# Kernel optimization log

Measured on AMD Instinct MI355X. Metric: run time of the kernel, lower is better.

The kernel has to match this reference:

```python
import jax, jax.numpy as jnp
import numpy as np

B, T, H = 2, 2048, 1024
EXPAND, N = 2, 16
DIN = H * EXPAND  # 2048
EPS = 1e-6


def rmsnorm(x, w):
    var = jnp.mean(x * x, axis=-1, keepdims=True)
    return x * jax.lax.rsqrt(var + EPS) * w


def setup_inputs() -> dict:
    key = jax.random.key(0)
    ks = jax.random.split(key, 9)
    s_h = 1.0 / np.sqrt(H)
    s_d = 1.0 / np.sqrt(DIN)
    return {
        "x": jax.random.normal(ks[0], (B, T, H), jnp.float32),
        "norm_w": jnp.ones((H,), jnp.float32),
        "in_proj_w": jax.random.normal(ks[1], (H, 2 * DIN), jnp.float32) * s_h,
        "A_proj_w": jax.random.normal(ks[2], (DIN, DIN), jnp.float32) * s_d,
        "A_proj_b": jax.random.normal(ks[3], (DIN,), jnp.float32) * 0.02,
        "A_base": jnp.log(jnp.arange(1, N + 1, dtype=jnp.float32)),
        "B_proj_w": jax.random.normal(ks[4], (DIN, N), jnp.float32) * s_d,
        "C_proj_w": jax.random.normal(ks[5], (DIN, N), jnp.float32) * s_d,
        "D": jnp.ones((DIN,), jnp.float32),
        "out_proj_w": jax.random.normal(ks[6], (DIN, H), jnp.float32) * s_d,
    }


def liquid_scan(x_in, a_mod, a_base, B_in, C_in):
    # x_in, a_mod: [B,T,DIN]; B_in, C_in: [B,T,N]; a_base: [N]
    def step(h, inp):
        a_t, b_t, c_t, x_t = inp  # [B,DIN], [B,N], [B,N], [B,DIN]
        # h: [B, DIN, N]
        h = (a_t[:, :, None] * a_base) * h + b_t[:, None, :] * x_t[:, :, None]
        y_t = jnp.einsum('bdn,bn->bd', h, c_t)
        return h, y_t

    h0 = jnp.zeros((x_in.shape[0], DIN, N), x_in.dtype)
    xs = (jnp.swapaxes(a_mod, 0, 1), jnp.swapaxes(B_in, 0, 1),
          jnp.swapaxes(C_in, 0, 1), jnp.swapaxes(x_in, 0, 1))
    _, ys = jax.lax.scan(step, h0, xs)  # ys: [T,B,DIN]
    return jnp.swapaxes(ys, 0, 1)


def reference(x, norm_w, in_proj_w, A_proj_w, A_proj_b, A_base, B_proj_w, C_proj_w, D, out_proj_w):
    residual = x
    xn = rmsnorm(x, norm_w)
    xz = xn @ in_proj_w                      # [B,T,2*DIN]
    x_in, z = jnp.split(xz, 2, axis=-1)
    x_in = jax.nn.silu(x_in)
    a_mod = jax.nn.sigmoid(x_in @ A_proj_w + A_proj_b)  # [B,T,DIN]
    a_base = jax.nn.sigmoid(A_base)                      # [N]
    B_in = x_in @ B_proj_w                               # [B,T,N]
    C_in = x_in @ C_proj_w                               # [B,T,N]
    y = liquid_scan(x_in, a_mod, a_base, B_in, C_in)     # [B,T,DIN]
    y = (y + D * x_in) * jax.nn.silu(z)
    return residual + y @ out_proj_w
```

## Files before the change

### kernel.cpp

```cpp
#include <hip/hip_runtime.h>
#include <hip/hip_fp16.h>
#include <cstdint>

#define B_    2
#define T_    2048
#define H_    1024
#define DIN_  2048
#define NS_   16
#define M_    (B_*T_)
#define NCHUNK 64
#define LCHUNK 32

using bf16x8 = __attribute__((ext_vector_type(8))) short;
using f32x4  = __attribute__((ext_vector_type(4))) float;

__device__ __forceinline__ unsigned short f2bf(float f) {
    union { float f; uint32_t u; } x; x.f = f;
    uint32_t u = x.u;
    uint32_t r = (u + 0x7fffu + ((u >> 16) & 1u)) >> 16;
    return (unsigned short)r;
}
__device__ __forceinline__ float bf2f(unsigned short h) {
    union { uint32_t u; float f; } x; x.u = ((uint32_t)h) << 16;
    return x.f;
}
__device__ __forceinline__ float sigm(float v) { return 1.0f / (1.0f + expf(-v)); }
__device__ __forceinline__ float silu(float v) { return v / (1.0f + expf(-v)); }

__device__ __forceinline__ void gload_lds16(const void* g, void* l) {
    __builtin_amdgcn_global_load_lds(
        (__attribute__((address_space(1))) void*)(void*)g,
        (__attribute__((address_space(3))) void*)l, 16, 0, 0);
}

__global__ __launch_bounds__(256)
void prep_weights(const float* __restrict__ in_proj, const float* __restrict__ A_proj,
                  const float* __restrict__ out_proj,
                  unsigned short* __restrict__ inT, unsigned short* __restrict__ W2,
                  unsigned short* __restrict__ outT) {
    int bid = blockIdx.x;
    int tid = threadIdx.x;
    const float* src; unsigned short* dst; int K, N, l;
    if (bid < 4096)      { src = in_proj;  dst = inT;  K = 1024; N = 4096; l = bid; }
    else if (bid < 8192) { src = A_proj;   dst = W2;   K = 2048; N = 2048; l = bid - 4096; }
    else                 { src = out_proj; dst = outT; K = 2048; N = 1024; l = bid - 8192; }
    int ntiles = N >> 5;
    int n0 = (l % ntiles) * 32, k0 = (l / ntiles) * 32;
    __shared__ float tile[32][33];
    int tx = tid & 31, ty = tid >> 5;
#pragma unroll
    for (int i = 0; i < 32; i += 8)
        tile[ty + i][tx] = src[(size_t)(k0 + ty + i) * N + (n0 + tx)];
    __syncthreads();
    int sx = (tid & 15) * 2;
    int sy = tid >> 4;
#pragma unroll
    for (int i = 0; i < 32; i += 16) {
        int n = sy + i;
        float v0 = tile[sx][n], v1 = tile[sx + 1][n];
        size_t o = (size_t)(n0 + n) * K + (k0 + sx);
        *(ushort2*)&dst[o] = make_ushort2(f2bf(v0), f2bf(v1));
    }
}

__global__ __launch_bounds__(256)
void rmsnorm_bf(const float* __restrict__ x, const float* __restrict__ w,
                unsigned short* __restrict__ xh) {
    int row = blockIdx.x;
    int tid = threadIdx.x;
    const float4* xr = (const float4*)(x + (size_t)row * H_);
    float4 v = xr[tid];
    float ss = v.x * v.x + v.y * v.y + v.z * v.z + v.w * v.w;
#pragma unroll
    for (int o = 32; o > 0; o >>= 1) ss += __shfl_down(ss, o, 64);
    __shared__ float red[4];
    int lane = tid & 63, wv = tid >> 6;
    if (lane == 0) red[wv] = ss;
    __syncthreads();
    float tot = red[0] + red[1] + red[2] + red[3];
    float rstd = rsqrtf(tot / (float)H_ + 1e-6f);
    const float4* wr = (const float4*)w;
    float4 w4 = wr[tid];
    size_t o = (size_t)row * H_ + tid * 4;
    *(ushort4*)&xh[o] = make_ushort4(f2bf(v.x * rstd * w4.x), f2bf(v.y * rstd * w4.y),
                                     f2bf(v.z * rstd * w4.z), f2bf(v.w * rstd * w4.w));
}

template <int EPI, int TM, int TN, int MW, int NW>
__global__ __launch_bounds__(512, 2)
void gemm_bf(const unsigned short* __restrict__ Aa, const unsigned short* __restrict__ Bw,
             int K,
             float* __restrict__ out0,
             unsigned short* __restrict__ oh, unsigned short* __restrict__ oz,
             const float* __restrict__ aux, __half* __restrict__ oha) {
    constexpr int UA    = (TM / 16) * 2;
    constexpr int UB    = (TN / 16) * 2;
    constexpr int UNITS = UA + UB;
    constexpr int SPW   = UNITS / 8;
    constexpr int MF    = TM / MW / 16;
    constexpr int NF    = TN / NW / 16;
    __shared__ unsigned short sm[3][UNITS * 512];
    const int tid  = threadIdx.x;
    const int lane = tid & 63;
    const int wid  = tid >> 6;
    const int wm   = wid / NW;
    const int wn   = wid % NW;

    const int gx   = gridDim.x;
    const int nwg  = gx * gridDim.y;
    const int orig = blockIdx.y * gx + blockIdx.x;
    const int qq   = nwg >> 3;
    const int lid  = (orig & 7) * qq + (orig >> 3);
    const int bm   = (lid / gx) * TM;
    const int bn   = (lid % gx) * TN;

    const unsigned short* b0 = Aa + (size_t)bm * K;
    const unsigned short* b1 = Bw + (size_t)bn * K;
    const int srow  = lane >> 2;
    const int sgran = (lane & 3) ^ ((lane >> 3) & 3);
    const unsigned short* gp[SPW];
    int lofs[SPW];
#pragma unroll
    for (int j = 0; j < SPW; ++j) {
        int u = wid * SPW + j;
        int rel = (u < UA) ? u : (u - UA);
        const unsigned short* base = (u < UA) ? b0 : b1;
        int chunk = rel >> 1, ks = rel & 1;
        gp[j] = base + (size_t)(chunk * 16 + srow) * K + ks * 32 + sgran * 8;
        lofs[j] = u * 512;
    }

    const int nt = K >> 6;
#pragma unroll
    for (int j = 0; j < SPW; ++j) gload_lds16(gp[j], &sm[0][lofs[j]]);
#pragma unroll
    for (int j = 0; j < SPW; ++j) gload_lds16(gp[j] + 64, &sm[1][lofs[j]]);

    const int fro = (lane & 15) * 32 + (((lane >> 4) ^ ((lane >> 1) & 3)) * 8);

    f32x4 acc[MF][NF] = {};
    int bsel = 0;
    for (int kt = 0; kt < nt; ++kt) {
        if (kt + 1 < nt) {
            if constexpr (SPW == 6)      asm volatile("s_waitcnt vmcnt(6)" ::: "memory");
            else if constexpr (SPW == 4) asm volatile("s_waitcnt vmcnt(4)" ::: "memory");
            else                         asm volatile("s_waitcnt vmcnt(8)" ::: "memory");
        } else {
            asm volatile("s_waitcnt vmcnt(0)" ::: "memory");
        }
        __builtin_amdgcn_s_barrier();
        __builtin_amdgcn_sched_barrier(0);
        int nb = bsel + 2; if (nb >= 3) nb -= 3;
        const unsigned short* sb = sm[bsel];
        const bool pf = (kt + 2 < nt);
#pragma unroll
        for (int ks = 0; ks < 2; ++ks) {
            bf16x8 af[MF], bf8[NF];
#pragma unroll
            for (int mf = 0; mf < MF; ++mf)
                af[mf] = *(const bf16x8*)&sb[((wm * MF + mf) * 2 + ks) * 512 + fro];
#pragma unroll
            for (int nf = 0; nf < NF; ++nf)
                bf8[nf] = *(const bf16x8*)&sb[(UA + (wn * NF + nf) * 2 + ks) * 512 + fro];
            if (pf) {
#pragma unroll
                for (int j = 0; j < SPW / 2; ++j) {
                    int jj = ks * (SPW / 2) + j;
                    gload_lds16(gp[jj] + (size_t)(kt + 2) * 64, &sm[nb][lofs[jj]]);
                }
            }
            __builtin_amdgcn_s_setprio(1);
#pragma unroll
            for (int mf = 0; mf < MF; ++mf)
#pragma unroll
                for (int nf = 0; nf < NF; ++nf)
                    acc[mf][nf] = __builtin_amdgcn_mfma_f32_16x16x32_bf16(af[mf], bf8[nf], acc[mf][nf], 0, 0, 0);
            __builtin_amdgcn_s_setprio(0);
            if (ks == 0) {
                __builtin_amdgcn_s_barrier();
                __builtin_amdgcn_sched_barrier(0);
            }
        }
        bsel += 1; if (bsel == 3) bsel = 0;
    }

#pragma unroll
    for (int mf = 0; mf < MF; ++mf)
#pragma unroll
        for (int nf = 0; nf < NF; ++nf) {
            int col  = bn + (wn * NF + nf) * 16 + (lane & 15);
            int row0 = bm + (wm * MF + mf) * 16 + ((lane >> 4) << 2);
#pragma unroll
            for (int r = 0; r < 4; ++r) {
                int row = row0 + r;
                float v = acc[mf][nf][r];
                if (EPI == 0) {
                    float s = silu(v);
                    if (col < DIN_) oh[(size_t)row * DIN_ + col] = f2bf(s);
                    else            oz[(size_t)row * DIN_ + (col - DIN_)] = f2bf(s);
                } else if (EPI == 1) {
                    oha[(size_t)row * DIN_ + col] = __float2half(sigm(v + aux[col]));
                } else {
                    out0[(size_t)row * H_ + col] = v + aux[(size_t)row * H_ + col];
                }
            }
        }
}

#define KT_ 512
__global__ __launch_bounds__(256)
void bc_proj(const unsigned short* __restrict__ xh,
             const float* __restrict__ Bw, const float* __restrict__ Cw,
             float* __restrict__ Bout, float* __restrict__ Cout) {
    __shared__ float wB[KT_][17];
    __shared__ float wC[KT_][17];
    const int m0  = blockIdx.x * 16;
    const int tid = threadIdx.x;
    const int r   = tid >> 4;
    const int j   = tid & 15;
    float ab[16], ac[16];
#pragma unroll
    for (int i = 0; i < 16; ++i) { ab[i] = 0.f; ac[i] = 0.f; }

    for (int kt = 0; kt < DIN_; kt += KT_) {
        if (kt) __syncthreads();
        const float4* bs = (const float4*)(Bw + (size_t)kt * 16);
        const float4* cs = (const float4*)(Cw + (size_t)kt * 16);
#pragma unroll
        for (int i = 0; i < 8; ++i) {
            int idx = i * 256 + tid;
            int kk = idx >> 2, c4 = (idx & 3) * 4;
            float4 vb = bs[idx], vc = cs[idx];
            wB[kk][c4 + 0] = vb.x; wB[kk][c4 + 1] = vb.y; wB[kk][c4 + 2] = vb.z; wB[kk][c4 + 3] = vb.w;
            wC[kk][c4 + 0] = vc.x; wC[kk][c4 + 1] = vc.y; wC[kk][c4 + 2] = vc.z; wC[kk][c4 + 3] = vc.w;
        }
        __syncthreads();
        const unsigned short* xr = xh + (size_t)(m0 + r) * DIN_ + kt;
#pragma unroll 4
        for (int kk = 0; kk < 32; ++kk) {
            int kl = kk * 16 + j;
            float x = bf2f(xr[kl]);
#pragma unroll
            for (int c = 0; c < 16; ++c) {
                ab[c] = fmaf(x, wB[kl][c], ab[c]);
                ac[c] = fmaf(x, wC[kl][c], ac[c]);
            }
        }
    }
#pragma unroll
    for (int i = 0; i < 16; ++i) {
#pragma unroll
        for (int m = 8; m > 0; m >>= 1) {
            ab[i] += __shfl_xor(ab[i], m, 64);
            ac[i] += __shfl_xor(ac[i], m, 64);
        }
    }
    if (j == 0) {
#pragma unroll
        for (int i = 0; i < 16; ++i) {
            Bout[(size_t)(m0 + r) * 16 + i] = ab[i];
            Cout[(size_t)(m0 + r) * 16 + i] = ac[i];
        }
    }
}

__global__ __launch_bounds__(256)
void scan_phase1(const __half* __restrict__ amod, const unsigned short* __restrict__ xh,
                 const float* __restrict__ Bin, const float* __restrict__ Abase,
                 float* __restrict__ P, float* __restrict__ S) {
    int d = blockIdx.x * 256 + threadIdx.x;
    int c = blockIdx.y;
    int b = blockIdx.z;
    float ab[16];
#pragma unroll
    for (int n = 0; n < 16; ++n) ab[n] = sigm(Abase[n]);
    float p[16], s[16];
#pragma unroll
    for (int n = 0; n < 16; ++n) { p[n] = 1.0f; s[n] = 0.0f; }
    int t0 = c * LCHUNK;
    for (int tt = 0; tt < LCHUNK; ++tt) {
        size_t mrow = (size_t)(b * T_ + t0 + tt);
        float a = __half2float(amod[mrow * DIN_ + d]);
        float x = bf2f(xh[mrow * DIN_ + d]);
        const float4* bt4 = (const float4*)(Bin + mrow * 16);
        float4 q0 = bt4[0], q1 = bt4[1], q2 = bt4[2], q3 = bt4[3];
        float bt[16];
        bt[0]=q0.x; bt[1]=q0.y; bt[2]=q0.z; bt[3]=q0.w;
        bt[4]=q1.x; bt[5]=q1.y; bt[6]=q1.z; bt[7]=q1.w;
        bt[8]=q2.x; bt[9]=q2.y; bt[10]=q2.z; bt[11]=q2.w;
        bt[12]=q3.x; bt[13]=q3.y; bt[14]=q3.z; bt[15]=q3.w;
#pragma unroll
        for (int n = 0; n < 16; ++n) {
            float dk = a * ab[n];
            p[n] *= dk;
            s[n] = fmaf(dk, s[n], bt[n] * x);
        }
    }
    size_t base = ((size_t)(b * NCHUNK + c) << 15) + (size_t)d * 16;
    float4* P4 = (float4*)(P + base);
    float4* S4 = (float4*)(S + base);
#pragma unroll
    for (int j = 0; j < 4; ++j) {
        P4[j] = make_float4(p[4*j], p[4*j+1], p[4*j+2], p[4*j+3]);
        S4[j] = make_float4(s[4*j], s[4*j+1], s[4*j+2], s[4*j+3]);
    }
}

__global__ __launch_bounds__(256)
void scan_phase2(const float* __restrict__ P, const float* __restrict__ S,
                 float* __restrict__ H0) {
    int idx = blockIdx.x * 256 + threadIdx.x;
    int b = idx >> 15;
    int dn = idx & 32767;
    float g = 0.f;
    for (int c = 0; c < NCHUNK; ++c) {
        size_t base = ((size_t)(b * NCHUNK + c) << 15) + dn;
        H0[base] = g;
        g = fmaf(P[base], g, S[base]);
    }
}

__global__ __launch_bounds__(256)
void scan_phase3(const __half* __restrict__ amod, const unsigned short* __restrict__ xh,
                 const float* __restrict__ Bin, const float* __restrict__ Cin,
                 const float* __restrict__ Abase, const float* __restrict__ H0,
                 const float* __restrict__ Dp, const unsigned short* __restrict__ szh,
                 unsigned short* __restrict__ yh) {
    int d = blockIdx.x * 256 + threadIdx.x;
    int c = blockIdx.y;
    int b = blockIdx.z;
    float ab[16];
#pragma unroll
    for (int n = 0; n < 16; ++n) ab[n] = sigm(Abase[n]);
    float h[16];
    size_t hbase = ((size_t)(b * NCHUNK + c) << 15) + (size_t)d * 16;
    const float4* H4 = (const float4*)(H0 + hbase);
#pragma unroll
    for (int j = 0; j < 4; ++j) {
        float4 t4 = H4[j];
        h[j*4] = t4.x; h[j*4+1] = t4.y; h[j*4+2] = t4.z; h[j*4+3] = t4.w;
    }
    float Dd = Dp[d];
    int t0 = c * LCHUNK;
    for (int tt = 0; tt < LCHUNK; ++tt) {
        size_t mrow = (size_t)(b * T_ + t0 + tt);
        float a = __half2float(amod[mrow * DIN_ + d]);
        float x = bf2f(xh[mrow * DIN_ + d]);
        const float4* bt4 = (const float4*)(Bin + mrow * 16);
        const float4* ct4 = (const float4*)(Cin + mrow * 16);
        float4 q0 = bt4[0], q1 = bt4[1], q2 = bt4[2], q3 = bt4[3];
        float4 r0 = ct4[0], r1 = ct4[1], r2 = ct4[2], r3 = ct4[3];
        float bt[16], ct[16];
        bt[0]=q0.x; bt[1]=q0.y; bt[2]=q0.z; bt[3]=q0.w;
        bt[4]=q1.x; bt[5]=q1.y; bt[6]=q1.z; bt[7]=q1.w;
        bt[8]=q2.x; bt[9]=q2.y; bt[10]=q2.z; bt[11]=q2.w;
        bt[12]=q3.x; bt[13]=q3.y; bt[14]=q3.z; bt[15]=q3.w;
        ct[0]=r0.x; ct[1]=r0.y; ct[2]=r0.z; ct[3]=r0.w;
        ct[4]=r1.x; ct[5]=r1.y; ct[6]=r1.z; ct[7]=r1.w;
        ct[8]=r2.x; ct[9]=r2.y; ct[10]=r2.z; ct[11]=r2.w;
        ct[12]=r3.x; ct[13]=r3.y; ct[14]=r3.z; ct[15]=r3.w;
        float y = 0.f;
#pragma unroll
        for (int n = 0; n < 16; ++n) {
            float dk = a * ab[n];
            h[n] = fmaf(dk, h[n], bt[n] * x);
            y = fmaf(h[n], ct[n], y);
        }
        float val = (y + Dd * x) * bf2f(szh[mrow * DIN_ + d]);
        yh[mrow * DIN_ + d] = f2bf(val);
    }
}

extern "C" void kernel_launch(void* const* d_in, const int* in_sizes, int n_in,
                              void* d_out, int out_size, void* d_ws, size_t ws_size,
                              hipStream_t stream) {
    const float* x          = (const float*)d_in[0];
    const float* norm_w     = (const float*)d_in[1];
    const float* in_proj_w  = (const float*)d_in[2];
    const float* A_proj_w   = (const float*)d_in[3];
    const float* A_proj_b   = (const float*)d_in[4];
    const float* A_base     = (const float*)d_in[5];
    const float* B_proj_w   = (const float*)d_in[6];
    const float* C_proj_w   = (const float*)d_in[7];
    const float* Dp         = (const float*)d_in[8];
    const float* out_proj_w = (const float*)d_in[9];
    float* out = (float*)d_out;

    char* ws = (char*)d_ws;
    size_t off = 0;
    auto alloc = [&](size_t bytes) -> char* {
        char* p = ws + off;
        off += (bytes + 255) & ~(size_t)255;
        return p;
    };
    unsigned short* inT  = (unsigned short*)alloc((size_t)4096 * 1024 * 2);
    unsigned short* W2   = (unsigned short*)alloc((size_t)2048 * 2048 * 2);
    unsigned short* outT = (unsigned short*)alloc((size_t)1024 * 2048 * 2);
    unsigned short* xnh  = (unsigned short*)alloc((size_t)M_ * H_ * 2);
    unsigned short* xinh = (unsigned short*)alloc((size_t)M_ * DIN_ * 2);
    unsigned short* szh  = (unsigned short*)alloc((size_t)M_ * DIN_ * 2);
    __half* amod  = (__half*)alloc((size_t)M_ * DIN_ * 2);
    float* Bin    = (float*)alloc((size_t)M_ * 16 * 4);
    float* Cin    = (float*)alloc((size_t)M_ * 16 * 4);
    float* Pw     = (float*)alloc((size_t)B_ * NCHUNK * DIN_ * NS_ * 4);
    float* Sw     = (float*)alloc((size_t)B_ * NCHUNK * DIN_ * NS_ * 4);
    float* H0w    = (float*)alloc((size_t)B_ * NCHUNK * DIN_ * NS_ * 4);
    unsigned short* yh = (unsigned short*)alloc((size_t)M_ * DIN_ * 2);
    (void)ws_size;

    prep_weights<<<10240, 256, 0, stream>>>(in_proj_w, A_proj_w, out_proj_w, inT, W2, outT);

    rmsnorm_bf<<<M_, 256, 0, stream>>>(x, norm_w, xnh);

    gemm_bf<0, 256, 128, 2, 4><<<dim3(4096 / 128, M_ / 256), 512, 0, stream>>>(
        xnh, inT, 1024, nullptr, xinh, szh, nullptr, nullptr);

    gemm_bf<1, 256, 128, 2, 4><<<dim3(2048 / 128, M_ / 256), 512, 0, stream>>>(
        xinh, W2, 2048, nullptr, nullptr, nullptr, A_proj_b, amod);

    bc_proj<<<M_ / 16, 256, 0, stream>>>(xinh, B_proj_w, C_proj_w, Bin, Cin);

    scan_phase1<<<dim3(DIN_ / 256, NCHUNK, B_), 256, 0, stream>>>(amod, xinh, Bin, A_base, Pw, Sw);
    scan_phase2<<<(B_ * DIN_ * NS_) / 256, 256, 0, stream>>>(Pw, Sw, H0w);
    scan_phase3<<<dim3(DIN_ / 256, NCHUNK, B_), 256, 0, stream>>>(
        amod, xinh, Bin, Cin, A_base, H0w, Dp, szh, yh);

    gemm_bf<2, 128, 128, 2, 4><<<dim3(1024 / 128, M_ / 128), 512, 0, stream>>>(
        yh, outT, 2048, out, nullptr, nullptr, x, nullptr);
}
```

Baseline: 232.8 us.

## Rewrite GEMM pipeline as double-buffered with sub-phase barriers and larger tiles

Replaces the triple-buffered bf16 GEMM with a double-buffered variant that issues prefetches for the next k-tile in finer sub-phases, each separated by its own barrier, with explicit lgkmcnt waits before the MFMAs. It also enlarges the in_proj tile to 256x256 and raises occupancy hints for the 128x128 tile. The aim is to cut LDS footprint so more workgroups fit per CU and to interleave loads with MFMAs more evenly. The cost is more barriers per k-step and a shorter prefetch distance, which may expose global load latency.

Result: no change. 230.8 us (-0.9%).

```diff
diff --git a/kernel.cpp b/kernel.cpp
--- a/kernel.cpp
+++ b/kernel.cpp
@@ -86,102 +86,114 @@
                                      f2bf(v.z * rstd * w4.z), f2bf(v.w * rstd * w4.w));
 }
 
-template <int EPI, int TM, int TN, int MW, int NW>
-__global__ __launch_bounds__(512, 2)
-void gemm_bf(const unsigned short* __restrict__ Aa, const unsigned short* __restrict__ Bw,
-             int K,
-             float* __restrict__ out0,
-             unsigned short* __restrict__ oh, unsigned short* __restrict__ oz,
-             const float* __restrict__ aux, __half* __restrict__ oha) {
-    constexpr int UA    = (TM / 16) * 2;
-    constexpr int UB    = (TN / 16) * 2;
-    constexpr int UNITS = UA + UB;
-    constexpr int SPW   = UNITS / 8;
-    constexpr int MF    = TM / MW / 16;
-    constexpr int NF    = TN / NW / 16;
-    __shared__ unsigned short sm[3][UNITS * 512];
+template <int EPI, int BM, int BN>
+__global__ __launch_bounds__(512, (BM == 128) ? 4 : 2)
+void gemm8p(const unsigned short* __restrict__ Aa, const unsigned short* __restrict__ Bw,
+            int K,
+            float* __restrict__ out0,
+            unsigned short* __restrict__ oh, unsigned short* __restrict__ oz,
+            const float* __restrict__ aux, __half* __restrict__ oha) {
+    constexpr int AU   = (BM / 16) * 2;
+    constexpr int BU   = (BN / 16) * 2;
+    constexpr int BUFU = AU + BU;
+    constexpr int MF   = BM / 2 / 16;
+    constexpr int NF   = BN / 4 / 16;
+    constexpr int PH   = (NF == 4) ? 2 : 1;
+    constexpr int NP   = NF / PH;
+    constexpr int SPWK = BUFU / 8;
+    constexpr int SPG  = SPWK / 2;
+    constexpr int SPP  = SPG / PH;
+    __shared__ unsigned short sm[2 * BUFU * 512];
     const int tid  = threadIdx.x;
     const int lane = tid & 63;
     const int wid  = tid >> 6;
-    const int wm   = wid / NW;
-    const int wn   = wid % NW;
+    const int wm   = wid >> 2;
+    const int wn   = wid & 3;
 
     const int gx   = gridDim.x;
     const int nwg  = gx * gridDim.y;
     const int orig = blockIdx.y * gx + blockIdx.x;
     const int qq   = nwg >> 3;
     const int lid  = (orig & 7) * qq + (orig >> 3);
-    const int bm   = (lid / gx) * TM;
-    const int bn   = (lid % gx) * TN;
-
-    const unsigned short* b0 = Aa + (size_t)bm * K;
-    const unsigned short* b1 = Bw + (size_t)bn * K;
+    const int bm   = (lid / gx) * BM;
+    const int bn   = (lid % gx) * BN;
+
     const int srow  = lane >> 2;
     const int sgran = (lane & 3) ^ ((lane >> 3) & 3);
-    const unsigned short* gp[SPW];
-    int lofs[SPW];
-#pragma unroll
-    for (int j = 0; j < SPW; ++j) {
-        int u = wid * SPW + j;
-        int rel = (u < UA) ? u : (u - UA);
-        const unsigned short* base = (u < UA) ? b0 : b1;
-        int chunk = rel >> 1, ks = rel & 1;
-        gp[j] = base + (size_t)(chunk * 16 + srow) * K + ks * 32 + sgran * 8;
-        lofs[j] = u * 512;
-    }
+    const unsigned short* gpp[SPWK];
+    int lofs_[SPWK];
+#pragma unroll
+    for (int g = 0; g < 2; ++g)
+#pragma unroll
+        for (int i = 0; i < SPG; ++i) {
+            int cn = wid * SPG + i;
+            const unsigned short* src;
+            int u;
+            if (cn < AU / 2) { u = cn * 2 + g;             src = Aa + (size_t)(bm + cn * 16 + srow) * K; }
+            else { int bc = cn - AU / 2; u = AU + bc * 2 + g; src = Bw + (size_t)(bn + bc * 16 + srow) * K; }
+            gpp[g * SPG + i]   = src + g * 32 + sgran * 8;
+            lofs_[g * SPG + i] = u * 512;
+        }
 
     const int nt = K >> 6;
 #pragma unroll
-    for (int j = 0; j < SPW; ++j) gload_lds16(gp[j], &sm[0][lofs[j]]);
-#pragma unroll
-    for (int j = 0; j < SPW; ++j) gload_lds16(gp[j] + 64, &sm[1][lofs[j]]);
+    for (int j = 0; j < SPWK; ++j) gload_lds16(gpp[j], &sm[lofs_[j]]);
 
     const int fro = (lane & 15) * 32 + (((lane >> 4) ^ ((lane >> 1) & 3)) * 8);
 
     f32x4 acc[MF][NF] = {};
-    int bsel = 0;
     for (int kt = 0; kt < nt; ++kt) {
-        if (kt + 1 < nt) {
-            if constexpr (SPW == 6)      asm volatile("s_waitcnt vmcnt(6)" ::: "memory");
-            else if constexpr (SPW == 4) asm volatile("s_waitcnt vmcnt(4)" ::: "memory");
-            else                         asm volatile("s_waitcnt vmcnt(8)" ::: "memory");
-        } else {
-            asm volatile("s_waitcnt vmcnt(0)" ::: "memory");
-        }
-        __builtin_amdgcn_s_barrier();
-        __builtin_amdgcn_sched_barrier(0);
-        int nb = bsel + 2; if (nb >= 3) nb -= 3;
-        const unsigned short* sb = sm[bsel];
-        const bool pf = (kt + 2 < nt);
+        const unsigned short* sb = &sm[(kt & 1) * (BUFU * 512)];
+        unsigned short*       db = &sm[((kt + 1) & 1) * (BUFU * 512)];
+        const bool pf = (kt + 1 < nt);
+        bf16x8 af[MF];
 #pragma unroll
         for (int ks = 0; ks < 2; ++ks) {
-            bf16x8 af[MF], bf8[NF];
-#pragma unroll
-            for (int mf = 0; mf < MF; ++mf)
-                af[mf] = *(const bf16x8*)&sb[((wm * MF + mf) * 2 + ks) * 512 + fro];
-#pragma unroll
-            for (int nf = 0; nf < NF; ++nf)
-                bf8[nf] = *(const bf16x8*)&sb[(UA + (wn * NF + nf) * 2 + ks) * 512 + fro];
-            if (pf) {
-#pragma unroll
-                for (int j = 0; j < SPW / 2; ++j) {
-                    int jj = ks * (SPW / 2) + j;
-                    gload_lds16(gp[jj] + (size_t)(kt + 2) * 64, &sm[nb][lofs[jj]]);
+            if (ks == 1 && kt == nt - 1) {
+                asm volatile("s_waitcnt vmcnt(0)" ::: "memory");
+            } else {
+                if constexpr (SPG == 4)      asm volatile("s_waitcnt vmcnt(4)" ::: "memory");
+                else if constexpr (SPG == 3) asm volatile("s_waitcnt vmcnt(3)" ::: "memory");
+                else                         asm volatile("s_waitcnt vmcnt(2)" ::: "memory");
+            }
+            __builtin_amdgcn_s_barrier();
+            __builtin_amdgcn_sched_barrier(0);
+#pragma unroll
+            for (int ph = 0; ph < PH; ++ph) {
+                if (ph) {
+                    __builtin_amdgcn_s_barrier();
+                    __builtin_amdgcn_sched_barrier(0);
                 }
+                if (ph == 0) {
+#pragma unroll
+                    for (int mf = 0; mf < MF; ++mf)
+                        af[mf] = *(const bf16x8*)&sb[((wm * MF + mf) * 2 + ks) * 512 + fro];
+                }
+                bf16x8 bf8[NP];
+#pragma unroll
+                for (int j = 0; j < NP; ++j) {
+                    int nfg = ph * NP + j;
+                    bf8[j] = *(const bf16x8*)&sb[(AU + (wn * NF + nfg) * 2 + ks) * 512 + fro];
+                }
+                if (pf) {
+#pragma unroll
+                    for (int j = 0; j < SPP; ++j) {
+                        int s = (ks * PH + ph) * SPP + j;
+                        gload_lds16(gpp[s] + (size_t)(kt + 1) * 64, db + lofs_[s]);
+                    }
+                }
+                asm volatile("s_waitcnt lgkmcnt(0)" ::: "memory");
+                __builtin_amdgcn_sched_barrier(0);
+                __builtin_amdgcn_s_setprio(1);
+#pragma unroll
+                for (int mf = 0; mf < MF; ++mf)
+#pragma unroll
+                    for (int j = 0; j < NP; ++j)
+                        acc[mf][ph * NP + j] = __builtin_amdgcn_mfma_f32_16x16x32_bf16(
+                            af[mf], bf8[j], acc[mf][ph * NP + j], 0, 0, 0);
+                __builtin_amdgcn_s_setprio(0);
             }
-            __builtin_amdgcn_s_setprio(1);
-#pragma unroll
-            for (int mf = 0; mf < MF; ++mf)
-#pragma unroll
-                for (int nf = 0; nf < NF; ++nf)
-                    acc[mf][nf] = __builtin_amdgcn_mfma_f32_16x16x32_bf16(af[mf], bf8[nf], acc[mf][nf], 0, 0, 0);
-            __builtin_amdgcn_s_setprio(0);
-            if (ks == 0) {
-                __builtin_amdgcn_s_barrier();
-                __builtin_amdgcn_sched_barrier(0);
-            }
-        }
-        bsel += 1; if (bsel == 3) bsel = 0;
+        }
     }
 
 #pragma unroll
@@ -412,10 +424,10 @@
 
     rmsnorm_bf<<<M_, 256, 0, stream>>>(x, norm_w, xnh);
 
-    gemm_bf<0, 256, 128, 2, 4><<<dim3(4096 / 128, M_ / 256), 512, 0, stream>>>(
+    gemm8p<0, 256, 256><<<dim3(4096 / 256, M_ / 256), 512, 0, stream>>>(
         xnh, inT, 1024, nullptr, xinh, szh, nullptr, nullptr);
 
-    gemm_bf<1, 256, 128, 2, 4><<<dim3(2048 / 128, M_ / 256), 512, 0, stream>>>(
+    gemm8p<1, 256, 128><<<dim3(2048 / 128, M_ / 256), 512, 0, stream>>>(
         xinh, W2, 2048, nullptr, nullptr, nullptr, A_proj_b, amod);
 
     bc_proj<<<M_ / 16, 256, 0, stream>>>(xinh, B_proj_w, C_proj_w, Bin, Cin);
@@ -425,6 +437,6 @@
     scan_phase3<<<dim3(DIN_ / 256, NCHUNK, B_), 256, 0, stream>>>(
         amod, xinh, Bin, Cin, A_base, H0w, Dp, szh, yh);
 
-    gemm_bf<2, 128, 128, 2, 4><<<dim3(1024 / 128, M_ / 128), 512, 0, stream>>>(
+    gemm8p<2, 128, 128><<<dim3(1024 / 128, M_ / 128), 512, 0, stream>>>(
         yh, outT, 2048, out, nullptr, nullptr, x, nullptr);
 }
```
